# Kernel optimization log

Measured on AMD Instinct MI355X. Metric: run time of the kernel, lower is better.

The kernel has to match this reference:

```python
import jax, jax.numpy as jnp
import numpy as np

NUM_LAYERS = 4
N_HEADS = 16
D_MODEL = 1024
D_FF = 4096
K = 7
L = 2048
C_IN = 4
C_OUT = 4
HD = D_MODEL // N_HEADS  # 64
EPS = 1e-5
THETA = 10000.0


def setup_inputs() -> dict:
    key = jax.random.key(0)
    ks = iter(jax.random.split(key, 32))

    def rn(shape, scale=0.02):
        return jax.random.normal(next(ks), shape, jnp.float32) * scale

    return {
        "x": jax.random.normal(next(ks), (C_IN, L), jnp.float32),
        "conv_in_w": rn((D_MODEL, C_IN, K)),
        "conv_in_b": rn((D_MODEL,)),
        "ln1_w": jnp.ones((NUM_LAYERS, D_MODEL), jnp.float32),
        "ln1_b": jnp.zeros((NUM_LAYERS, D_MODEL), jnp.float32),
        "wq": rn((NUM_LAYERS, D_MODEL, D_MODEL)),
        "wk": rn((NUM_LAYERS, D_MODEL, D_MODEL)),
        "wv": rn((NUM_LAYERS, D_MODEL, D_MODEL)),
        "wo": rn((NUM_LAYERS, D_MODEL, D_MODEL)),
        "ln2_w": jnp.ones((NUM_LAYERS, D_MODEL), jnp.float32),
        "ln2_b": jnp.zeros((NUM_LAYERS, D_MODEL), jnp.float32),
        "w1": rn((NUM_LAYERS, D_FF, D_MODEL)),
        "b1": rn((NUM_LAYERS, D_FF)),
        "w2": rn((NUM_LAYERS, D_FF, D_FF)),
        "b2": rn((NUM_LAYERS, D_FF)),
        "w3": rn((NUM_LAYERS, D_MODEL, D_FF)),
        "b3": rn((NUM_LAYERS, D_MODEL)),
        "conv_out_w": rn((C_OUT, D_MODEL, K)),
        "conv_out_b": rn((C_OUT,)),
    }


def conv1d_causal(x, w, b):
    # x: [C_in, L]; w: [C_out, C_in, K]; causal left-pad (K-1, 0)
    xp = jnp.pad(x, ((0, 0), (K - 1, 0)))[None]  # [1, C_in, L+K-1]
    y = jax.lax.conv_general_dilated(xp, w, (1,), "VALID", dimension_numbers=("NCH", "OIH", "NCH"))[0]
    return y + b[:, None]


def rms_norm(x, w, b):
    # eqx.nn.RMSNorm with weight and bias, applied per token
    inv = jax.lax.rsqrt(jnp.mean(x * x, axis=-1, keepdims=True) + EPS)
    return x * inv * w + b


def rope(x):
    # x: [L, H, HD]; eqx RotaryPositionalEmbedding (rotate-half / NeoX style)
    seq = x.shape[0]
    freqs = 1.0 / (THETA ** (jnp.arange(0, HD, 2, dtype=jnp.float32) / HD))  # [HD/2]
    ang = jnp.arange(seq, dtype=jnp.float32)[:, None] * freqs[None, :]  # [L, HD/2]
    cos = jnp.tile(jnp.cos(ang), (1, 2))[:, None, :]  # [L, 1, HD]
    sin = jnp.tile(jnp.sin(ang), (1, 2))[:, None, :]
    x1, x2 = jnp.split(x, 2, axis=-1)
    rot = jnp.concatenate((-x2, x1), axis=-1)
    return x * cos + rot * sin


def block(x, ln1_w, ln1_b, wq, wk, wv, wo, ln2_w, ln2_b, w1, b1, w2, b2, w3, b3):
    seq = x.shape[0]
    h = rms_norm(x, ln1_w, ln1_b)
    q = (h @ wq.T).reshape(seq, N_HEADS, HD)
    k = (h @ wk.T).reshape(seq, N_HEADS, HD)
    v = (h @ wv.T).reshape(seq, N_HEADS, HD)
    q = rope(q)
    k = rope(k)
    scores = jnp.einsum("shd,Shd->hsS", q / jnp.sqrt(jnp.float32(HD)), k)  # [H, L, L]
    causal = jnp.tril(jnp.ones((seq, seq), bool))
    scores = jnp.where(causal[None], scores, jnp.finfo(scores.dtype).min)
    attn = jax.nn.softmax(scores, axis=-1)
    o = jnp.einsum("hsS,Shd->shd", attn, v).reshape(seq, D_MODEL)
    x = x + o @ wo.T
    # eqx.nn.MLP depth=2: Linear->relu->Linear->relu->Linear
    h = rms_norm(x, ln2_w, ln2_b)
    h = jax.nn.relu(h @ w1.T + b1)
    h = jax.nn.relu(h @ w2.T + b2)
    return x + h @ w3.T + b3


def _forward(x, conv_in_w, conv_in_b, ln1_w, ln1_b, wq, wk, wv, wo, ln2_w, ln2_b, w1, b1, w2, b2, w3, b3, conv_out_w, conv_out_b):
    h = jax.nn.relu(conv1d_causal(x, conv_in_w, conv_in_b))  # [D_MODEL, L]
    h = h.T  # [L, D_MODEL]
    for i in range(NUM_LAYERS):
        h = block(h, ln1_w[i], ln1_b[i], wq[i], wk[i], wv[i], wo[i], ln2_w[i], ln2_b[i], w1[i], b1[i], w2[i], b2[i], w3[i], b3[i])
    h = h.T  # [D_MODEL, L]
    return conv1d_causal(h, conv_out_w, conv_out_b)  # [C_OUT, L]


def reference(x, conv_in_w, conv_in_b, ln1_w, ln1_b, wq, wk, wv, wo, ln2_w, ln2_b, w1, b1, w2, b2, w3, b3, conv_out_w, conv_out_b):
    return _forward(x, conv_in_w, conv_in_b, ln1_w, ln1_b, wq, wk, wv, wo, ln2_w, ln2_b, w1, b1, w2, b2, w3, b3, conv_out_w, conv_out_b)
```

## Files before the change

### kernel.cpp

```cpp
#include <hip/hip_runtime.h>
#include <math.h>

#define L_SEQ 2048
#define DM 1024
#define DFF 4096
#define NH 16
#define HD 64

typedef __bf16 bf16_t;
typedef __bf16 bf16x4 __attribute__((ext_vector_type(4)));
typedef __bf16 bf16x8 __attribute__((ext_vector_type(8)));
typedef float floatx4 __attribute__((ext_vector_type(4)));

__device__ __forceinline__ void gl_lds16(const void* g, void* l) {
    __builtin_amdgcn_global_load_lds((const __attribute__((address_space(1))) void*)g,
                                     (__attribute__((address_space(3))) void*)l, 16, 0, 0);
}

__global__ __launch_bounds__(256) void conv_in_kernel(const float* __restrict__ x,
                                                      const float* __restrict__ w,
                                                      const float* __restrict__ b,
                                                      float* __restrict__ h) {
    int gid = blockIdx.x * 256 + threadIdx.x;
    int d = gid & (DM - 1);
    int l = gid >> 10;
    float acc = b[d];
    const float* wd = w + d * 28;
#pragma unroll
    for (int c = 0; c < 4; ++c) {
#pragma unroll
        for (int k = 0; k < 7; ++k) {
            int t = l + k - 6;
            float xv = (t >= 0) ? x[c * L_SEQ + t] : 0.f;
            acc = fmaf(xv, wd[c * 7 + k], acc);
        }
    }
    h[(size_t)l * DM + d] = fmaxf(acc, 0.f);
}

__global__ __launch_bounds__(256) void rmsnorm_kernel(const float* __restrict__ h,
                                                      const float* __restrict__ w,
                                                      const float* __restrict__ b,
                                                      bf16_t* __restrict__ out) {
    int l = blockIdx.x;
    int t = threadIdx.x;
    const float* row = h + (size_t)l * DM;
    float4 xv = *(const float4*)(row + t * 4);
    float ss = xv.x * xv.x + xv.y * xv.y + xv.z * xv.z + xv.w * xv.w;
#pragma unroll
    for (int off = 1; off < 64; off <<= 1) ss += __shfl_xor(ss, off, 64);
    __shared__ float red[4];
    if ((t & 63) == 0) red[t >> 6] = ss;
    __syncthreads();
    float tot = red[0] + red[1] + red[2] + red[3];
    float inv = rsqrtf(tot * (1.f / DM) + 1e-5f);
    float4 wv = *(const float4*)(w + t * 4);
    float4 bv = *(const float4*)(b + t * 4);
    bf16x4 ov;
    ov.x = (bf16_t)fmaf(xv.x * inv, wv.x, bv.x);
    ov.y = (bf16_t)fmaf(xv.y * inv, wv.y, bv.y);
    ov.z = (bf16_t)fmaf(xv.z * inv, wv.z, bv.z);
    ov.w = (bf16_t)fmaf(xv.w * inv, wv.w, bv.w);
    *(bf16x4*)(out + (size_t)l * DM + t * 4) = ov;
}

__global__ __launch_bounds__(256) void cvt_bf16(const float* __restrict__ in,
                                                bf16_t* __restrict__ out, int n4) {
    int i = blockIdx.x * 256 + threadIdx.x;
    if (i < n4) {
        float4 v = *(const float4*)(in + (size_t)i * 4);
        bf16x4 o = {(bf16_t)v.x, (bf16_t)v.y, (bf16_t)v.z, (bf16_t)v.w};
        *(bf16x4*)(out + (size_t)i * 4) = o;
    }
}

__global__ __launch_bounds__(256) void cvt_qkvw(const float* __restrict__ wq,
                                                const float* __restrict__ wk,
                                                const float* __restrict__ wv,
                                                bf16_t* __restrict__ out) {
    int i = blockIdx.x * 256 + threadIdx.x;
    int layer = i / 786432;
    int rem = i - layer * 786432;
    int sel = rem / 262144;
    int idx = rem - sel * 262144;
    const float* src = (sel == 0 ? wq : sel == 1 ? wk : wv) + (size_t)layer * 1048576 + (size_t)idx * 4;
    float4 v = *(const float4*)src;
    bf16x4 o = {(bf16_t)v.x, (bf16_t)v.y, (bf16_t)v.z, (bf16_t)v.w};
    *(bf16x4*)(out + (size_t)i * 4) = o;
}

template <bool BIAS, bool RELU, bool RES, bool OUTBF>
__global__ __launch_bounds__(256, 2) void gemm_pl(const bf16_t* __restrict__ A,
                                                  const bf16_t* __restrict__ B,
                                                  const float* __restrict__ bias,
                                                  const float* __restrict__ res,
                                                  void* __restrict__ Cout,
                                                  int M, int N, int K) {
    __shared__ alignas(16) char smem[32768];
    const int t = threadIdx.x;
    const int w = t >> 6;
    const int lane = t & 63;
    const int quad = lane >> 4;
    const int l16 = lane & 15;
    const int bm = blockIdx.y * 128;
    const int bn = blockIdx.x * 128;
    const int wm = (w >> 1) * 64;
    const int wn = (w & 1) * 64;

    const int swz = (quad ^ ((l16 >> 1) & 3)) << 4;
    int aoff[4], boff[4];
#pragma unroll
    for (int i = 0; i < 4; ++i) {
        aoff[i] = (wm + i * 16 + l16) * 64 + swz;
        boff[i] = 8192 + (wn + i * 16 + l16) * 64 + swz;
    }

    const int srow = w * 16 + (lane >> 2);
    const int scl = (((lane & 3) ^ ((lane >> 3) & 3)) << 4);
    const char* pA = (const char*)(A + (size_t)(bm + srow) * K) + scl;
    const char* pB = (const char*)(B + (size_t)(bn + srow) * K) + scl;
    const size_t rK = (size_t)K * 128;
    const int ldw = w * 1024;

    const int NT = K >> 5;

    floatx4 acc[4][4];
#pragma unroll
    for (int i = 0; i < 4; ++i)
#pragma unroll
        for (int j = 0; j < 4; ++j) acc[i][j] = (floatx4)0.f;

#pragma unroll
    for (int tt = 0; tt < 2; ++tt) {
        char* lb = smem + tt * 16384;
        gl_lds16(pA + (size_t)tt * 64, lb + ldw);
        gl_lds16(pA + (size_t)tt * 64 + rK, lb + ldw + 4096);
        gl_lds16(pB + (size_t)tt * 64, lb + 8192 + ldw);
        gl_lds16(pB + (size_t)tt * 64 + rK, lb + 8192 + ldw + 4096);
    }
    asm volatile("s_waitcnt vmcnt(4)" ::: "memory");
    __builtin_amdgcn_s_barrier();

    for (int tile = 0; tile < NT; ++tile) {
        char* cb = smem + (tile & 1) * 16384;
        const bool st = (tile + 2) < NT;
        const size_t gof = (size_t)(tile + 2) * 64;

        bf16x8 af[4], bfr[4];
#pragma unroll
        for (int i = 0; i < 4; ++i) af[i] = *(const bf16x8*)(cb + aoff[i]);
#pragma unroll
        for (int j = 0; j < 4; ++j) bfr[j] = *(const bf16x8*)(cb + boff[j]);
        asm volatile("s_waitcnt lgkmcnt(0)" ::: "memory");
        __builtin_amdgcn_sched_barrier(0);
        __builtin_amdgcn_s_barrier();

        if (st) {
            gl_lds16(pA + gof, cb + ldw);
            gl_lds16(pA + gof + rK, cb + ldw + 4096);
            gl_lds16(pB + gof, cb + 8192 + ldw);
            gl_lds16(pB + gof + rK, cb + 8192 + ldw + 4096);
        }

        __builtin_amdgcn_s_setprio(1);
#pragma unroll
        for (int i = 0; i < 4; ++i)
#pragma unroll
            for (int j = 0; j < 4; ++j)
                acc[i][j] = __builtin_amdgcn_mfma_f32_16x16x32_bf16(af[i], bfr[j], acc[i][j], 0, 0, 0);
        __builtin_amdgcn_s_setprio(0);

        if (st) asm volatile("s_waitcnt vmcnt(4)" ::: "memory");
        else    asm volatile("s_waitcnt vmcnt(0)" ::: "memory");
        __builtin_amdgcn_s_barrier();
    }

#pragma unroll
    for (int j = 0; j < 4; ++j) {
        const int n = bn + wn + j * 16 + l16;
        const float bv = BIAS ? bias[n] : 0.f;
#pragma unroll
        for (int i = 0; i < 4; ++i) {
            const int m = bm + wm + i * 16 + quad * 4;
#pragma unroll
            for (int r = 0; r < 4; ++r) {
                float v = acc[i][j][r] + bv;
                if (RELU) v = fmaxf(v, 0.f);
                if (RES) v += res[(size_t)(m + r) * N + n];
                if (OUTBF) ((bf16_t*)Cout)[(size_t)(m + r) * N + n] = (bf16_t)v;
                else ((float*)Cout)[(size_t)(m + r) * N + n] = v;
            }
        }
    }
}

__global__ __launch_bounds__(256) void rope_kernel(bf16_t* __restrict__ qkv) {
    int gid = blockIdx.x * 256 + threadIdx.x;
    int j = gid & 31;
    int hh = (gid >> 5) & 15;
    int l = gid >> 9;
    float freq = powf(10000.f, -(float)(2 * j) * (1.f / 64.f));
    float ang = (float)l * freq;
    float s = sinf(ang), c = cosf(ang);
    size_t base = (size_t)l * 3072 + hh * HD + j;
    float q1 = (float)qkv[base], q2 = (float)qkv[base + 32];
    qkv[base] = (bf16_t)(q1 * c - q2 * s);
    qkv[base + 32] = (bf16_t)(q2 * c + q1 * s);
    size_t kb = base + 1024;
    float k1 = (float)qkv[kb], k2 = (float)qkv[kb + 32];
    qkv[kb] = (bf16_t)(k1 * c - k2 * s);
    qkv[kb + 32] = (bf16_t)(k2 * c + k1 * s);
}

__global__ __launch_bounds__(256) void v_transpose(const bf16_t* __restrict__ qkvb,
                                                   bf16_t* __restrict__ vt) {
    __shared__ bf16_t Ts[64 * 72];
    const int h = blockIdx.x;
    const int tt = blockIdx.y;
    const int t = threadIdx.x;
#pragma unroll
    for (int i = 0; i < 2; ++i) {
        int idx = t + i * 256;
        int row = idx >> 3, dg = idx & 7;
        *(bf16x8*)(Ts + row * 72 + dg * 8) =
            *(const bf16x8*)(qkvb + (size_t)(tt * 64 + row) * 3072 + 2048 + h * 64 + dg * 8);
    }
    __syncthreads();
#pragma unroll
    for (int i = 0; i < 2; ++i) {
        int idx = t + i * 256;
        int d = idx >> 3, tg = idx & 7;
        bf16x8 v;
#pragma unroll
        for (int s = 0; s < 8; ++s) v[s] = Ts[(tg * 8 + s) * 72 + d];
        *(bf16x8*)(vt + ((size_t)h * 64 + d) * 2048 + tt * 64 + tg * 8) = v;
    }
}

__global__ __launch_bounds__(256) void attn_mfma(const bf16_t* __restrict__ qkvb,
                                                 const bf16_t* __restrict__ vt,
                                                 bf16_t* __restrict__ o) {
    __shared__ alignas(16) bf16_t Qs[64 * 72];
    __shared__ alignas(16) bf16_t Ks[64 * 72];
    __shared__ alignas(16) bf16_t Vs[64 * 72];
    __shared__ alignas(16) bf16_t Ps[4][16 * 72];
    const int t = threadIdx.x;
    const int wave = t >> 6;
    const int lane = t & 63;
    const int quad = lane >> 4;
    const int l16 = lane & 15;
    const int h = blockIdx.x;
    const int y = blockIdx.y;
    const int qt = (y < 16) ? (31 - y) : (y - 16);
    const int l0 = qt * 64;

#pragma unroll
    for (int i = 0; i < 2; ++i) {
        int idx = t + i * 256;
        int row = idx >> 3, dg = idx & 7;
        *(bf16x8*)(Qs + row * 72 + dg * 8) =
            *(const bf16x8*)(qkvb + (size_t)(l0 + row) * 3072 + h * HD + dg * 8);
    }

    float m_r[4], l_r[4];
    floatx4 acc_o[4];
#pragma unroll
    for (int r = 0; r < 4; ++r) { m_r[r] = -1e30f; l_r[r] = 0.f; }
#pragma unroll
    for (int n = 0; n < 4; ++n) acc_o[n] = (floatx4)0.f;

    for (int jt = 0; jt <= qt; ++jt) {
        const int j0 = jt * 64;
        __syncthreads();
#pragma unroll
        for (int i = 0; i < 2; ++i) {
            int idx = t + i * 256;
            int row = idx >> 3, dg = idx & 7;
            *(bf16x8*)(Ks + row * 72 + dg * 8) =
                *(const bf16x8*)(qkvb + (size_t)(j0 + row) * 3072 + 1024 + h * HD + dg * 8);
            *(bf16x8*)(Vs + row * 72 + dg * 8) =
                *(const bf16x8*)(vt + ((size_t)h * HD + row) * 2048 + j0 + dg * 8);
        }
        __syncthreads();

        bf16x8 aq0 = *(const bf16x8*)(Qs + (wave * 16 + l16) * 72 + quad * 8);
        bf16x8 aq1 = *(const bf16x8*)(Qs + (wave * 16 + l16) * 72 + 32 + quad * 8);
        floatx4 sacc[4];
#pragma unroll
        for (int j = 0; j < 4; ++j) {
            bf16x8 bk0 = *(const bf16x8*)(Ks + (j * 16 + l16) * 72 + quad * 8);
            bf16x8 bk1 = *(const bf16x8*)(Ks + (j * 16 + l16) * 72 + 32 + quad * 8);
            floatx4 s = (floatx4)0.f;
            s = __builtin_amdgcn_mfma_f32_16x16x32_bf16(aq0, bk0, s, 0, 0, 0);
            s = __builtin_amdgcn_mfma_f32_16x16x32_bf16(aq1, bk1, s, 0, 0, 0);
            sacc[j] = s;
        }

        const bool diag = (jt == qt);
        float mt[4];
#pragma unroll
        for (int r = 0; r < 4; ++r) mt[r] = -1e30f;
#pragma unroll
        for (int j = 0; j < 4; ++j)
#pragma unroll
            for (int r = 0; r < 4; ++r) {
                float sv = sacc[j][r] * 0.125f;
                if (diag && (j * 16 + l16) > (wave * 16 + quad * 4 + r)) sv = -1e30f;
                sacc[j][r] = sv;
                mt[r] = fmaxf(mt[r], sv);
            }
#pragma unroll
        for (int r = 0; r < 4; ++r) {
            mt[r] = fmaxf(mt[r], __shfl_xor(mt[r], 1, 64));
            mt[r] = fmaxf(mt[r], __shfl_xor(mt[r], 2, 64));
            mt[r] = fmaxf(mt[r], __shfl_xor(mt[r], 4, 64));
            mt[r] = fmaxf(mt[r], __shfl_xor(mt[r], 8, 64));
        }
        float alpha[4], rs[4];
#pragma unroll
        for (int r = 0; r < 4; ++r) {
            float mn = fmaxf(m_r[r], mt[r]);
            alpha[r] = __expf(m_r[r] - mn);
            m_r[r] = mn;
            rs[r] = 0.f;
        }
#pragma unroll
        for (int j = 0; j < 4; ++j)
#pragma unroll
            for (int r = 0; r < 4; ++r) {
                float p = __expf(sacc[j][r] - m_r[r]);
                sacc[j][r] = p;
                rs[r] += p;
            }
#pragma unroll
        for (int r = 0; r < 4; ++r) {
            rs[r] += __shfl_xor(rs[r], 1, 64);
            rs[r] += __shfl_xor(rs[r], 2, 64);
            rs[r] += __shfl_xor(rs[r], 4, 64);
            rs[r] += __shfl_xor(rs[r], 8, 64);
            l_r[r] = l_r[r] * alpha[r] + rs[r];
        }
#pragma unroll
        for (int n = 0; n < 4; ++n)
#pragma unroll
            for (int r = 0; r < 4; ++r) acc_o[n][r] *= alpha[r];

        bf16_t* pw = Ps[wave];
#pragma unroll
        for (int j = 0; j < 4; ++j)
#pragma unroll
            for (int r = 0; r < 4; ++r)
                pw[(quad * 4 + r) * 72 + j * 16 + l16] = (bf16_t)sacc[j][r];

        bf16x8 ap0 = *(const bf16x8*)(pw + l16 * 72 + quad * 8);
        bf16x8 ap1 = *(const bf16x8*)(pw + l16 * 72 + 32 + quad * 8);
#pragma unroll
        for (int n = 0; n < 4; ++n) {
            bf16x8 bv0 = *(const bf16x8*)(Vs + (n * 16 + l16) * 72 + quad * 8);
            bf16x8 bv1 = *(const bf16x8*)(Vs + (n * 16 + l16) * 72 + 32 + quad * 8);
            acc_o[n] = __builtin_amdgcn_mfma_f32_16x16x32_bf16(ap0, bv0, acc_o[n], 0, 0, 0);
            acc_o[n] = __builtin_amdgcn_mfma_f32_16x16x32_bf16(ap1, bv1, acc_o[n], 0, 0, 0);
        }
    }

#pragma unroll
    for (int r = 0; r < 4; ++r) {
        float inv = 1.f / l_r[r];
        int row = l0 + wave * 16 + quad * 4 + r;
#pragma unroll
        for (int n = 0; n < 4; ++n)
            o[(size_t)row * DM + h * HD + n * 16 + l16] = (bf16_t)(acc_o[n][r] * inv);
    }
}

__global__ __launch_bounds__(256) void conv_out_kernel(const float* __restrict__ h,
                                                       const float* __restrict__ w,
                                                       const float* __restrict__ b,
                                                       float* __restrict__ out) {
    int c = blockIdx.x >> 11;
    int l = blockIdx.x & 2047;
    int t = threadIdx.x;
    float acc = 0.f;
    const float* wc = w + c * (DM * 7);
    for (int idx = t; idx < DM * 7; idx += 256) {
        int d = idx / 7;
        int kk = idx - d * 7;
        int tt = l + kk - 6;
        if (tt >= 0) acc = fmaf(h[(size_t)tt * DM + d], wc[idx], acc);
    }
#pragma unroll
    for (int off = 1; off < 64; off <<= 1) acc += __shfl_xor(acc, off, 64);
    __shared__ float red[4];
    if ((t & 63) == 0) red[t >> 6] = acc;
    __syncthreads();
    if (t == 0) out[blockIdx.x] = red[0] + red[1] + red[2] + red[3] + b[c];
}

extern "C" void kernel_launch(void* const* d_in, const int* in_sizes, int n_in,
                              void* d_out, int out_size, void* d_ws, size_t ws_size,
                              hipStream_t stream) {
    const float* x = (const float*)d_in[0];
    const float* conv_in_w = (const float*)d_in[1];
    const float* conv_in_b = (const float*)d_in[2];
    const float* ln1_w = (const float*)d_in[3];
    const float* ln1_b = (const float*)d_in[4];
    const float* wq = (const float*)d_in[5];
    const float* wk = (const float*)d_in[6];
    const float* wv = (const float*)d_in[7];
    const float* wo = (const float*)d_in[8];
    const float* ln2_w = (const float*)d_in[9];
    const float* ln2_b = (const float*)d_in[10];
    const float* w1 = (const float*)d_in[11];
    const float* b1 = (const float*)d_in[12];
    const float* w2 = (const float*)d_in[13];
    const float* b2 = (const float*)d_in[14];
    const float* w3 = (const float*)d_in[15];
    const float* b3 = (const float*)d_in[16];
    const float* conv_out_w = (const float*)d_in[17];
    const float* conv_out_b = (const float*)d_in[18];

    char* W = (char*)d_ws;
    float* h = (float*)(W);
    bf16_t* qkvb = (bf16_t*)(W + (8ull << 20));
    bf16_t* hn = (bf16_t*)(W + (20ull << 20));
    bf16_t* ob = (bf16_t*)(W + (24ull << 20));
    bf16_t* f1 = (bf16_t*)(W + (28ull << 20));
    bf16_t* f2 = (bf16_t*)(W + (44ull << 20));
    bf16_t* vtb = (bf16_t*)(W + (60ull << 20));
    bf16_t* qkvw = (bf16_t*)(W + (64ull << 20));
    bf16_t* wob = (bf16_t*)(W + (88ull << 20));
    bf16_t* w1b = (bf16_t*)(W + (96ull << 20));
    bf16_t* w2b = (bf16_t*)(W + (128ull << 20));
    bf16_t* w3b = (bf16_t*)(W + (256ull << 20));

    cvt_qkvw<<<12288, 256, 0, stream>>>(wq, wk, wv, qkvw);
    cvt_bf16<<<4096, 256, 0, stream>>>(wo, wob, 1048576);
    cvt_bf16<<<16384, 256, 0, stream>>>(w1, w1b, 4194304);
    cvt_bf16<<<65536, 256, 0, stream>>>(w2, w2b, 16777216);
    cvt_bf16<<<16384, 256, 0, stream>>>(w3, w3b, 4194304);

    conv_in_kernel<<<(L_SEQ * DM) / 256, 256, 0, stream>>>(x, conv_in_w, conv_in_b, h);

    for (int layer = 0; layer < 4; ++layer) {
        const float* ln1w = ln1_w + layer * DM;
        const float* ln1b = ln1_b + layer * DM;
        const float* ln2w = ln2_w + layer * DM;
        const float* ln2b = ln2_b + layer * DM;
        const bf16_t* qkvw_l = qkvw + (size_t)layer * 3072 * 1024;
        const bf16_t* wob_l = wob + (size_t)layer * DM * DM;
        const bf16_t* w1b_l = w1b + (size_t)layer * DFF * DM;
        const bf16_t* w2b_l = w2b + (size_t)layer * DFF * DFF;
        const bf16_t* w3b_l = w3b + (size_t)layer * DM * DFF;
        const float* b1_l = b1 + (size_t)layer * DFF;
        const float* b2_l = b2 + (size_t)layer * DFF;
        const float* b3_l = b3 + (size_t)layer * DM;

        rmsnorm_kernel<<<L_SEQ, 256, 0, stream>>>(h, ln1w, ln1b, hn);
        gemm_pl<false, false, false, true><<<dim3(3072 / 128, L_SEQ / 128), 256, 0, stream>>>(
            hn, qkvw_l, nullptr, nullptr, qkvb, L_SEQ, 3072, 1024);
        rope_kernel<<<(L_SEQ * NH * 32) / 256, 256, 0, stream>>>(qkvb);
        v_transpose<<<dim3(NH, L_SEQ / 64), 256, 0, stream>>>(qkvb, vtb);
        attn_mfma<<<dim3(NH, L_SEQ / 64), 256, 0, stream>>>(qkvb, vtb, ob);
        gemm_pl<false, false, true, false><<<dim3(DM / 128, L_SEQ / 128), 256, 0, stream>>>(
            ob, wob_l, nullptr, h, h, L_SEQ, DM, DM);
        rmsnorm_kernel<<<L_SEQ, 256, 0, stream>>>(h, ln2w, ln2b, hn);
        gemm_pl<true, true, false, true><<<dim3(DFF / 128, L_SEQ / 128), 256, 0, stream>>>(
            hn, w1b_l, b1_l, nullptr, f1, L_SEQ, DFF, 1024);
        gemm_pl<true, true, false, true><<<dim3(DFF / 128, L_SEQ / 128), 256, 0, stream>>>(
            f1, w2b_l, b2_l, nullptr, f2, L_SEQ, DFF, DFF);
        gemm_pl<true, false, true, false><<<dim3(DM / 128, L_SEQ / 128), 256, 0, stream>>>(
            f2, w3b_l, b3_l, h, h, L_SEQ, DM, DFF);
    }

    conv_out_kernel<<<4 * L_SEQ, 256, 0, stream>>>(h, conv_out_w, conv_out_b, (float*)d_out);
}
```

Before: 1.960 ms.

## Fuse fp32-to-bf16 weight conversion into GEMM B-tile loads

```diff
diff --git a/kernel.cpp b/kernel.cpp
--- a/kernel.cpp
+++ b/kernel.cpp
@@ -64,38 +64,15 @@
     *(bf16x4*)(out + (size_t)l * DM + t * 4) = ov;
 }
 
-__global__ __launch_bounds__(256) void cvt_bf16(const float* __restrict__ in,
-                                                bf16_t* __restrict__ out, int n4) {
-    int i = blockIdx.x * 256 + threadIdx.x;
-    if (i < n4) {
-        float4 v = *(const float4*)(in + (size_t)i * 4);
-        bf16x4 o = {(bf16_t)v.x, (bf16_t)v.y, (bf16_t)v.z, (bf16_t)v.w};
-        *(bf16x4*)(out + (size_t)i * 4) = o;
-    }
-}
-
-__global__ __launch_bounds__(256) void cvt_qkvw(const float* __restrict__ wq,
-                                                const float* __restrict__ wk,
-                                                const float* __restrict__ wv,
-                                                bf16_t* __restrict__ out) {
-    int i = blockIdx.x * 256 + threadIdx.x;
-    int layer = i / 786432;
-    int rem = i - layer * 786432;
-    int sel = rem / 262144;
-    int idx = rem - sel * 262144;
-    const float* src = (sel == 0 ? wq : sel == 1 ? wk : wv) + (size_t)layer * 1048576 + (size_t)idx * 4;
-    float4 v = *(const float4*)src;
-    bf16x4 o = {(bf16_t)v.x, (bf16_t)v.y, (bf16_t)v.z, (bf16_t)v.w};
-    *(bf16x4*)(out + (size_t)i * 4) = o;
-}
-
-template <bool BIAS, bool RELU, bool RES, bool OUTBF>
-__global__ __launch_bounds__(256, 2) void gemm_pl(const bf16_t* __restrict__ A,
-                                                  const bf16_t* __restrict__ B,
-                                                  const float* __restrict__ bias,
-                                                  const float* __restrict__ res,
-                                                  void* __restrict__ Cout,
-                                                  int M, int N, int K) {
+template <bool QKV3, bool BIAS, bool RELU, bool RES, bool OUTBF>
+__global__ __launch_bounds__(256, 2) void gemm_plf(const bf16_t* __restrict__ A,
+                                                   const float* __restrict__ B0,
+                                                   const float* __restrict__ B1,
+                                                   const float* __restrict__ B2,
+                                                   const float* __restrict__ bias,
+                                                   const float* __restrict__ res,
+                                                   void* __restrict__ Cout,
+                                                   int M, int N, int K) {
     __shared__ alignas(16) char smem[32768];
     const int t = threadIdx.x;
     const int w = t >> 6;
@@ -118,10 +95,23 @@
     const int srow = w * 16 + (lane >> 2);
     const int scl = (((lane & 3) ^ ((lane >> 3) & 3)) << 4);
     const char* pA = (const char*)(A + (size_t)(bm + srow) * K) + scl;
-    const char* pB = (const char*)(B + (size_t)(bn + srow) * K) + scl;
     const size_t rK = (size_t)K * 128;
     const int ldw = w * 1024;
 
+    const int rB = t >> 1;
+    const int hB = t & 1;
+    const float* Bsel;
+    if (QKV3) {
+        const int sel = bn >> 10;
+        Bsel = (sel == 0 ? B0 : sel == 1 ? B1 : B2) + (size_t)(bn & 1023) * K;
+    } else {
+        Bsel = B0 + (size_t)bn * K;
+    }
+    const float* pBF = Bsel + (size_t)rB * K + hB * 16;
+    const int hashB = (rB >> 1) & 3;
+    const int bw0 = 8192 + rB * 64 + (((2 * hB) ^ hashB) << 4);
+    const int bw1 = 8192 + rB * 64 + (((2 * hB + 1) ^ hashB) << 4);
+
     const int NT = K >> 5;
 
     floatx4 acc[4][4];
@@ -130,21 +120,35 @@
 #pragma unroll
         for (int j = 0; j < 4; ++j) acc[i][j] = (floatx4)0.f;
 
+    float4 q0 = *(const float4*)(pBF + 0);
+    float4 q1 = *(const float4*)(pBF + 4);
+    float4 q2 = *(const float4*)(pBF + 8);
+    float4 q3 = *(const float4*)(pBF + 12);
+    __builtin_amdgcn_sched_barrier(0);
 #pragma unroll
     for (int tt = 0; tt < 2; ++tt) {
         char* lb = smem + tt * 16384;
         gl_lds16(pA + (size_t)tt * 64, lb + ldw);
         gl_lds16(pA + (size_t)tt * 64 + rK, lb + ldw + 4096);
-        gl_lds16(pB + (size_t)tt * 64, lb + 8192 + ldw);
-        gl_lds16(pB + (size_t)tt * 64 + rK, lb + 8192 + ldw + 4096);
-    }
-    asm volatile("s_waitcnt vmcnt(4)" ::: "memory");
+    }
+    asm volatile("s_waitcnt vmcnt(2)" ::: "memory");
+    {
+        bf16x8 lo, hi;
+        lo[0]=(bf16_t)q0.x; lo[1]=(bf16_t)q0.y; lo[2]=(bf16_t)q0.z; lo[3]=(bf16_t)q0.w;
+        lo[4]=(bf16_t)q1.x; lo[5]=(bf16_t)q1.y; lo[6]=(bf16_t)q1.z; lo[7]=(bf16_t)q1.w;
+        hi[0]=(bf16_t)q2.x; hi[1]=(bf16_t)q2.y; hi[2]=(bf16_t)q2.z; hi[3]=(bf16_t)q2.w;
+        hi[4]=(bf16_t)q3.x; hi[5]=(bf16_t)q3.y; hi[6]=(bf16_t)q3.z; hi[7]=(bf16_t)q3.w;
+        *(bf16x8*)(smem + bw0) = lo;
+        *(bf16x8*)(smem + bw1) = hi;
+    }
+    asm volatile("s_waitcnt lgkmcnt(0)" ::: "memory");
     __builtin_amdgcn_s_barrier();
 
     for (int tile = 0; tile < NT; ++tile) {
         char* cb = smem + (tile & 1) * 16384;
-        const bool st = (tile + 2) < NT;
-        const size_t gof = (size_t)(tile + 2) * 64;
+        char* nb = smem + ((tile + 1) & 1) * 16384;
+        const bool stA = (tile + 2) < NT;
+        const bool ldB = (tile + 1) < NT;
 
         bf16x8 af[4], bfr[4];
 #pragma unroll
@@ -155,11 +159,19 @@
         __builtin_amdgcn_sched_barrier(0);
         __builtin_amdgcn_s_barrier();
 
-        if (st) {
+        float4 p0, p1, p2, p3;
+        if (ldB) {
+            const float* src = pBF + (size_t)(tile + 1) * 32;
+            p0 = *(const float4*)(src + 0);
+            p1 = *(const float4*)(src + 4);
+            p2 = *(const float4*)(src + 8);
+            p3 = *(const float4*)(src + 12);
+        }
+        __builtin_amdgcn_sched_barrier(0);
+        if (stA) {
+            const size_t gof = (size_t)(tile + 2) * 64;
             gl_lds16(pA + gof, cb + ldw);
             gl_lds16(pA + gof + rK, cb + ldw + 4096);
-            gl_lds16(pB + gof, cb + 8192 + ldw);
-            gl_lds16(pB + gof + rK, cb + 8192 + ldw + 4096);
         }
 
         __builtin_amdgcn_s_setprio(1);
@@ -170,9 +182,19 @@
                 acc[i][j] = __builtin_amdgcn_mfma_f32_16x16x32_bf16(af[i], bfr[j], acc[i][j], 0, 0, 0);
         __builtin_amdgcn_s_setprio(0);
 
-        if (st) asm volatile("s_waitcnt vmcnt(4)" ::: "memory");
-        else    asm volatile("s_waitcnt vmcnt(0)" ::: "memory");
-        __builtin_amdgcn_s_barrier();
+        if (ldB) {
+            if (stA) asm volatile("s_waitcnt vmcnt(2)" ::: "memory");
+            else     asm volatile("s_waitcnt vmcnt(0)" ::: "memory");
+            bf16x8 lo, hi;
+            lo[0]=(bf16_t)p0.x; lo[1]=(bf16_t)p0.y; lo[2]=(bf16_t)p0.z; lo[3]=(bf16_t)p0.w;
+            lo[4]=(bf16_t)p1.x; lo[5]=(bf16_t)p1.y; lo[6]=(bf16_t)p1.z; lo[7]=(bf16_t)p1.w;
+            hi[0]=(bf16_t)p2.x; hi[1]=(bf16_t)p2.y; hi[2]=(bf16_t)p2.z; hi[3]=(bf16_t)p2.w;
+            hi[4]=(bf16_t)p3.x; hi[5]=(bf16_t)p3.y; hi[6]=(bf16_t)p3.z; hi[7]=(bf16_t)p3.w;
+            *(bf16x8*)(nb + bw0) = lo;
+            *(bf16x8*)(nb + bw1) = hi;
+            asm volatile("s_waitcnt lgkmcnt(0)" ::: "memory");
+            __builtin_amdgcn_s_barrier();
+        }
     }
 
 #pragma unroll
@@ -427,17 +449,6 @@
     bf16_t* f1 = (bf16_t*)(W + (28ull << 20));
     bf16_t* f2 = (bf16_t*)(W + (44ull << 20));
     bf16_t* vtb = (bf16_t*)(W + (60ull << 20));
-    bf16_t* qkvw = (bf16_t*)(W + (64ull << 20));
-    bf16_t* wob = (bf16_t*)(W + (88ull << 20));
-    bf16_t* w1b = (bf16_t*)(W + (96ull << 20));
-    bf16_t* w2b = (bf16_t*)(W + (128ull << 20));
-    bf16_t* w3b = (bf16_t*)(W + (256ull << 20));
-
-    cvt_qkvw<<<12288, 256, 0, stream>>>(wq, wk, wv, qkvw);
-    cvt_bf16<<<4096, 256, 0, stream>>>(wo, wob, 1048576);
-    cvt_bf16<<<16384, 256, 0, stream>>>(w1, w1b, 4194304);
-    cvt_bf16<<<65536, 256, 0, stream>>>(w2, w2b, 16777216);
-    cvt_bf16<<<16384, 256, 0, stream>>>(w3, w3b, 4194304);
 
     conv_in_kernel<<<(L_SEQ * DM) / 256, 256, 0, stream>>>(x, conv_in_w, conv_in_b, h);
 
@@ -446,30 +457,32 @@
         const float* ln1b = ln1_b + layer * DM;
         const float* ln2w = ln2_w + layer * DM;
         const float* ln2b = ln2_b + layer * DM;
-        const bf16_t* qkvw_l = qkvw + (size_t)layer * 3072 * 1024;
-        const bf16_t* wob_l = wob + (size_t)layer * DM * DM;
-        const bf16_t* w1b_l = w1b + (size_t)layer * DFF * DM;
-        const bf16_t* w2b_l = w2b + (size_t)layer * DFF * DFF;
-        const bf16_t* w3b_l = w3b + (size_t)layer * DM * DFF;
+        const float* wq_l = wq + (size_t)layer * DM * DM;
+        const float* wk_l = wk + (size_t)layer * DM * DM;
+        const float* wv_l = wv + (size_t)layer * DM * DM;
+        const float* wo_l = wo + (size_t)layer * DM * DM;
+        const float* w1_l = w1 + (size_t)layer * DFF * DM;
+        const float* w2_l = w2 + (size_t)layer * DFF * DFF;
+        const float* w3_l = w3 + (size_t)layer * DM * DFF;
         const float* b1_l = b1 + (size_t)layer * DFF;
         const float* b2_l = b2 + (size_t)layer * DFF;
         const float* b3_l = b3 + (size_t)layer * DM;
 
         rmsnorm_kernel<<<L_SEQ, 256, 0, stream>>>(h, ln1w, ln1b, hn);
-        gemm_pl<false, false, false, true><<<dim3(3072 / 128, L_SEQ / 128), 256, 0, stream>>>(
-            hn, qkvw_l, nullptr, nullptr, qkvb, L_SEQ, 3072, 1024);
+        gemm_plf<true, false, false, false, true><<<dim3(3072 / 128, L_SEQ / 128), 256, 0, stream>>>(
+            hn, wq_l, wk_l, wv_l, nullptr, nullptr, qkvb, L_SEQ, 3072, 1024);
         rope_kernel<<<(L_SEQ * NH * 32) / 256, 256, 0, stream>>>(qkvb);
         v_transpose<<<dim3(NH, L_SEQ / 64), 256, 0, stream>>>(qkvb, vtb);
         attn_mfma<<<dim3(NH, L_SEQ / 64), 256, 0, stream>>>(qkvb, vtb, ob);
-        gemm_pl<false, false, true, false><<<dim3(DM / 128, L_SEQ / 128), 256, 0, stream>>>(
-            ob, wob_l, nullptr, h, h, L_SEQ, DM, DM);
+        gemm_plf<false, false, false, true, false><<<dim3(DM / 128, L_SEQ / 128), 256, 0, stream>>>(
+            ob, wo_l, nullptr, nullptr, nullptr, h, h, L_SEQ, DM, DM);
         rmsnorm_kernel<<<L_SEQ, 256, 0, stream>>>(h, ln2w, ln2b, hn);
-        gemm_pl<true, true, false, true><<<dim3(DFF / 128, L_SEQ / 128), 256, 0, stream>>>(
-            hn, w1b_l, b1_l, nullptr, f1, L_SEQ, DFF, 1024);
-        gemm_pl<true, true, false, true><<<dim3(DFF / 128, L_SEQ / 128), 256, 0, stream>>>(
-            f1, w2b_l, b2_l, nullptr, f2, L_SEQ, DFF, DFF);
-        gemm_pl<true, false, true, false><<<dim3(DM / 128, L_SEQ / 128), 256, 0, stream>>>(
-            f2, w3b_l, b3_l, h, h, L_SEQ, DM, DFF);
+        gemm_plf<false, true, true, false, true><<<dim3(DFF / 128, L_SEQ / 128), 256, 0, stream>>>(
+            hn, w1_l, nullptr, nullptr, b1_l, nullptr, f1, L_SEQ, DFF, 1024);
+        gemm_plf<false, true, true, false, true><<<dim3(DFF / 128, L_SEQ / 128), 256, 0, stream>>>(
+            f1, w2_l, nullptr, nullptr, b2_l, nullptr, f2, L_SEQ, DFF, DFF);
+        gemm_plf<false, true, false, true, false><<<dim3(DM / 128, L_SEQ / 128), 256, 0, stream>>>(
+            f2, w3_l, nullptr, nullptr, b3_l, h, h, L_SEQ, DM, DFF);
     }
 
     conv_out_kernel<<<4 * L_SEQ, 256, 0, stream>>>(h, conv_out_w, conv_out_b, (float*)d_out);
```

After: 2.729 ms. 39.2% more time.
